# Optimization experiments

Hardware: AMD Instinct MI355X
Metric: run time of the kernel (lower is better)

Reference implementation:

```python
import jax, jax.numpy as jnp
import numpy as np

N, E = 20000, 640000
IN_CH, OUT_CH = 128, 64
HEADS = (4, 4)
NEG_SLOPE = 0.2


def _gat_layer(x, src, dst, edge_attr, edge_atten, W, a_src, a_dst, W_e, a_e, b, H, C, n_nodes):
    # x: [N, F_in] -> per-head features [N, H, C]
    xh = (x @ W).reshape(-1, H, C)
    alpha_src = jnp.sum(xh * a_src, axis=-1)          # [N, H]
    alpha_dst = jnp.sum(xh * a_dst, axis=-1)          # [N, H]
    eemb = (edge_attr @ W_e).reshape(-1, H, C)        # [E, H, C]
    alpha_e = jnp.sum(eemb * a_e, axis=-1)            # [E, H]
    alpha = alpha_src[src] + alpha_dst[dst] + alpha_e # [E, H]
    alpha = jax.nn.leaky_relu(alpha, NEG_SLOPE)
    # softmax over variable-degree neighborhoods (segments keyed by dst)
    amax = jax.ops.segment_max(alpha, dst, num_segments=n_nodes)
    alpha = jnp.exp(alpha - amax[dst])
    denom = jax.ops.segment_sum(alpha, dst, num_segments=n_nodes)
    alpha = alpha / (denom[dst] + 1e-16)
    msg = xh[src] * alpha[:, :, None]                 # [E, H, C]
    msg = msg * edge_atten[:, :, None]                # edge_atten: [E, 1] -> broadcast over H, C
    out = jax.ops.segment_sum(msg, dst, num_segments=n_nodes)
    out = out.reshape(n_nodes, H * C) + b
    return out, alpha


def setup_inputs() -> dict:
    key = jax.random.key(0)
    ks = jax.random.split(key, 16)
    H1, H2 = HEADS
    d1_in, d1_out = IN_CH, H1 * OUT_CH
    d2_in, d2_out = H1 * OUT_CH, H2 * OUT_CH
    s = lambda fi: 1.0 / np.sqrt(fi)
    inp = {
        "x": jax.random.normal(ks[0], (N, IN_CH), jnp.float32),
        "edge_index": jax.random.randint(ks[1], (2, E), 0, N, jnp.int64 if jax.config.jax_enable_x64 else jnp.int32),
        "batch": jnp.zeros((N,), jnp.int32),
        "edge_attr": jax.random.normal(ks[2], (E, 1), jnp.float32),
        "edge_atten": jax.random.uniform(ks[3], (E, 1), jnp.float32),
        # layer 1 params
        "W1": jax.random.normal(ks[4], (d1_in, d1_out), jnp.float32) * s(d1_in),
        "a_src1": jax.random.normal(ks[5], (H1, OUT_CH), jnp.float32) * s(OUT_CH),
        "a_dst1": jax.random.normal(ks[6], (H1, OUT_CH), jnp.float32) * s(OUT_CH),
        "W_e1": jax.random.normal(ks[7], (1, d1_out), jnp.float32),
        "a_e1": jax.random.normal(ks[8], (H1, OUT_CH), jnp.float32) * s(OUT_CH),
        "b1": jnp.zeros((d1_out,), jnp.float32),
        # layer 2 params
        "W2": jax.random.normal(ks[9], (d2_in, d2_out), jnp.float32) * s(d2_in),
        "a_src2": jax.random.normal(ks[10], (H2, OUT_CH), jnp.float32) * s(OUT_CH),
        "a_dst2": jax.random.normal(ks[11], (H2, OUT_CH), jnp.float32) * s(OUT_CH),
        "W_e2": jax.random.normal(ks[12], (1, d2_out), jnp.float32),
        "a_e2": jax.random.normal(ks[13], (H2, OUT_CH), jnp.float32) * s(OUT_CH),
        "b2": jnp.zeros((d2_out,), jnp.float32),
    }
    return inp


def reference(x, edge_index, batch, edge_attr, edge_atten,
              W1, a_src1, a_dst1, W_e1, a_e1, b1,
              W2, a_src2, a_dst2, W_e2, a_e2, b2):
    src, dst = edge_index[0], edge_index[1]
    h, w1 = _gat_layer(x, src, dst, edge_attr, edge_atten,
                       W1, a_src1, a_dst1, W_e1, a_e1, b1, HEADS[0], OUT_CH, N)
    h, w2 = _gat_layer(h, src, dst, edge_attr, edge_atten,
                       W2, a_src2, a_dst2, W_e2, a_e2, b2, HEADS[1], OUT_CH, N)
    return h, w1, w2
```

## Files before the change

kernel.cpp:

```cpp
#include <hip/hip_runtime.h>
#include <math.h>

#define NEG_SLOPE 0.2f
#define CAP 128
#define ST  136
#define NNODES 20000
#define NB 128

typedef short s16x8 __attribute__((ext_vector_type(8)));
typedef unsigned short us8 __attribute__((ext_vector_type(8)));
typedef float f32x4 __attribute__((ext_vector_type(4)));

__device__ __forceinline__ unsigned short f2bf(float f) {
    unsigned int u = __float_as_uint(f);
    return (unsigned short)((u + 0x7FFFu + ((u >> 16) & 1u)) >> 16);
}
__device__ __forceinline__ float bf2f(unsigned short s) {
    return __uint_as_float(((unsigned int)s) << 16);
}

__global__ __launch_bounds__(512) void hist_prep(const int* __restrict__ dst,
                                                 int* __restrict__ ghist,
                                                 int E, int chunk, int N, int histB,
                                                 const float* __restrict__ x,
                                                 const float* __restrict__ W1,
                                                 const float* __restrict__ W2,
                                                 const float* __restrict__ W_e1,
                                                 const float* __restrict__ a_e1,
                                                 const float* __restrict__ W_e2,
                                                 const float* __restrict__ a_e2,
                                                 unsigned short* __restrict__ xb16,
                                                 unsigned short* __restrict__ Wt1,
                                                 unsigned short* __restrict__ Wt2,
                                                 float* __restrict__ ce) {
    __shared__ int h[NNODES / 2];
    if ((int)blockIdx.x < histB) {
        const int b = blockIdx.x;
        const int NH = N >> 1;
        for (int i = threadIdx.x; i < NH; i += 512) h[i] = 0;
        __syncthreads();
        const int e0 = b * chunk;
        const int e1 = min(e0 + chunk, E);
        for (int e = e0 + (int)threadIdx.x; e < e1; e += 512) {
            int d = dst[e];
            atomicAdd(&h[d >> 1], 1 << ((d & 1) << 4));
        }
        __syncthreads();
        int2* out = (int2*)(ghist + (size_t)b * N);
        for (int i = threadIdx.x; i < NH; i += 512) {
            int v = h[i];
            out[i] = make_int2(v & 0xFFFF, ((unsigned)v) >> 16);
        }
    } else {
        const int p = (int)blockIdx.x - histB;
        const int gsz = 256 * 512;
        const int gid = p * 512 + (int)threadIdx.x;
        for (int i = gid; i < 128 * 256; i += gsz) {
            int k = i >> 8, n = i & 255;
            Wt1[n * 128 + k] = f2bf(W1[i]);
        }
        for (int i = gid; i < 256 * 256; i += gsz) {
            int k = i >> 8, n = i & 255;
            Wt2[n * 256 + k] = f2bf(W2[i]);
        }
        for (int i = gid; i < N * 32; i += gsz) {
            float4 f = ((const float4*)x)[i];
            ushort4 u = make_ushort4(f2bf(f.x), f2bf(f.y), f2bf(f.z), f2bf(f.w));
            ((ushort4*)xb16)[i] = u;
        }
        if (p < 2 && threadIdx.x < 256) {
            const float* We = p == 0 ? W_e1 : W_e2;
            const float* ae = p == 0 ? a_e1 : a_e2;
            int hh = threadIdx.x >> 6, c = threadIdx.x & 63;
            float pr = We[hh * 64 + c] * ae[hh * 64 + c];
#pragma unroll
            for (int off = 32; off > 0; off >>= 1) pr += __shfl_down(pr, off);
            if (c == 0) ce[p * 4 + hh] = pr;
        }
    }
}

__global__ __launch_bounds__(1024) void scan_kernel(const int* __restrict__ deg,
                                                    int* __restrict__ off, int N) {
    __shared__ int wsum[16];
    __shared__ int woff[16];
    __shared__ int s_carry, s_bt;
    if (threadIdx.x == 0) s_carry = 0;
    __syncthreads();
    const int lane = threadIdx.x & 63, wid = threadIdx.x >> 6;
    for (int base = 0; base < N; base += 4096) {
        int i0 = base + (int)threadIdx.x * 4;
        int v0 = (i0 + 0 < N) ? deg[i0 + 0] : 0;
        int v1 = (i0 + 1 < N) ? deg[i0 + 1] : 0;
        int v2 = (i0 + 2 < N) ? deg[i0 + 2] : 0;
        int v3 = (i0 + 3 < N) ? deg[i0 + 3] : 0;
        int tsum = v0 + v1 + v2 + v3;
        int incl = tsum;
#pragma unroll
        for (int ofs = 1; ofs < 64; ofs <<= 1) {
            int t = __shfl_up(incl, ofs);
            if (lane >= ofs) incl += t;
        }
        if (lane == 63) wsum[wid] = incl;
        __syncthreads();
        if (wid == 0) {
            int ws = (lane < 16) ? wsum[lane] : 0;
            int wincl = ws;
#pragma unroll
            for (int ofs = 1; ofs < 16; ofs <<= 1) {
                int t = __shfl_up(wincl, ofs);
                if (lane >= ofs) wincl += t;
            }
            if (lane < 16) woff[lane] = wincl - ws;
            if (lane == 15) s_bt = wincl;
        }
        __syncthreads();
        int e0 = s_carry + woff[wid] + incl - tsum;
        int e1 = e0 + v0, e2 = e1 + v1, e3 = e2 + v2;
        if (i0 + 0 < N) off[i0 + 0] = e0;
        if (i0 + 1 < N) off[i0 + 1] = e1;
        if (i0 + 2 < N) off[i0 + 2] = e2;
        if (i0 + 3 < N) off[i0 + 3] = e3;
        __syncthreads();
        if (threadIdx.x == 0) s_carry += s_bt;
        __syncthreads();
    }
    if (threadIdx.x == 0) off[N] = s_carry;
}

__device__ __forceinline__ void gemm_core(const unsigned short* __restrict__ A16,
                                          const unsigned short* __restrict__ Bt16,
                                          unsigned short* __restrict__ C16,
                                          const float* __restrict__ a_src,
                                          const float* __restrict__ a_dst,
                                          float* __restrict__ asrc,
                                          float* __restrict__ adst,
                                          int M, int K, int bx, int by,
                                          unsigned short (*As)[40],
                                          unsigned short (*Bs)[40]) {
    const int tid = threadIdx.x;
    const int w = tid >> 6, l = tid & 63;
    const int quad = l >> 4, m16 = l & 15;
    const int row0 = by * 128, col0 = bx * 64;

    f32x4 acc[2][4] = {};

    const int a_r = tid >> 1;
    const int a_k = (tid & 1) * 16;
    const int b_n = tid >> 2;
    const int b_k = (tid & 3) * 8;

    for (int k0 = 0; k0 < K; k0 += 32) {
        int gr = row0 + a_r; if (gr > M - 1) gr = M - 1;
        const unsigned short* ap = A16 + (size_t)gr * K + k0 + a_k;
        *(us8*)&As[a_r][a_k]     = *(const us8*)ap;
        *(us8*)&As[a_r][a_k + 8] = *(const us8*)(ap + 8);
        *(us8*)&Bs[b_n][b_k] = *(const us8*)(Bt16 + (size_t)(col0 + b_n) * K + k0 + b_k);
        __syncthreads();

        s16x8 af[2], bfr[4];
#pragma unroll
        for (int mt = 0; mt < 2; ++mt)
            af[mt] = *(const s16x8*)&As[w * 32 + mt * 16 + m16][quad * 8];
#pragma unroll
        for (int nt = 0; nt < 4; ++nt)
            bfr[nt] = *(const s16x8*)&Bs[nt * 16 + m16][quad * 8];
#pragma unroll
        for (int mt = 0; mt < 2; ++mt)
#pragma unroll
            for (int nt = 0; nt < 4; ++nt)
                acc[mt][nt] = __builtin_amdgcn_mfma_f32_16x16x32_bf16(af[mt], bfr[nt], acc[mt][nt], 0, 0, 0);
        __syncthreads();
    }

    const int h = bx;
    float was[4], wad[4];
#pragma unroll
    for (int nt = 0; nt < 4; ++nt) {
        int c = nt * 16 + m16;
        was[nt] = a_src[h * 64 + c];
        wad[nt] = a_dst[h * 64 + c];
    }

#pragma unroll
    for (int mt = 0; mt < 2; ++mt)
#pragma unroll
        for (int i = 0; i < 4; ++i) {
            int row = row0 + w * 32 + mt * 16 + quad * 4 + i;
            float ps = 0.f, pd = 0.f;
#pragma unroll
            for (int nt = 0; nt < 4; ++nt) {
                float v = acc[mt][nt][i];
                ps += v * was[nt];
                pd += v * wad[nt];
            }
#pragma unroll
            for (int ofs = 1; ofs < 16; ofs <<= 1) {
                ps += __shfl_xor(ps, ofs);
                pd += __shfl_xor(pd, ofs);
            }
            if (m16 == 0 && row < M) {
                asrc[(size_t)row * 4 + h] = ps;
                adst[(size_t)row * 4 + h] = pd;
            }
        }

#pragma unroll
    for (int mt = 0; mt < 2; ++mt)
#pragma unroll
        for (int nt = 0; nt < 4; ++nt) {
            int col = col0 + nt * 16 + m16;
#pragma unroll
            for (int i = 0; i < 4; ++i) {
                int row = row0 + w * 32 + mt * 16 + quad * 4 + i;
                if (row < M) C16[(size_t)row * 256 + col] = f2bf(acc[mt][nt][i]);
            }
        }
}

__global__ __launch_bounds__(256) void gemm1_scan(const unsigned short* __restrict__ A16,
                                                  const unsigned short* __restrict__ Bt16,
                                                  unsigned short* __restrict__ C16,
                                                  const float* __restrict__ a_src,
                                                  const float* __restrict__ a_dst,
                                                  float* __restrict__ asrc,
                                                  float* __restrict__ adst,
                                                  int M, int K, int gemmB,
                                                  int* __restrict__ ghist,
                                                  int* __restrict__ deg,
                                                  int N, int histB) {
    __shared__ unsigned short As[128][40];
    __shared__ unsigned short Bs[64][40];
    if ((int)blockIdx.x < gemmB) {
        gemm_core(A16, Bt16, C16, a_src, a_dst, asrc, adst, M, K,
                  blockIdx.x & 3, blockIdx.x >> 2, As, Bs);
    } else {
        int bin = ((int)blockIdx.x - gemmB) * 256 + (int)threadIdx.x;
        if (bin < N) {
            int run = 0;
            for (int b = 0; b < histB; b += 8) {
                int v[8];
#pragma unroll
                for (int j = 0; j < 8; ++j) v[j] = ghist[(b + j) * N + bin];
#pragma unroll
                for (int j = 0; j < 8; ++j) { ghist[(b + j) * N + bin] = run; run += v[j]; }
            }
            deg[bin] = run;
        }
    }
}

__global__ __launch_bounds__(1024) void fill2(const int* __restrict__ src,
                                              const int* __restrict__ dst,
                                              const float* __restrict__ edge_attr,
                                              const float* __restrict__ edge_atten,
                                              const int* __restrict__ off,
                                              const int* __restrict__ ghist,
                                              int4* __restrict__ rec,
                                              int E, int chunk, int N) {
    __shared__ int base[NNODES];
    const int b = blockIdx.x;
    const int* part = ghist + (size_t)b * N;
    for (int i = threadIdx.x; i < N; i += 1024) base[i] = off[i] + part[i];
    __syncthreads();
    const int e0 = b * chunk;
    const int e1 = min(e0 + chunk, E);
    for (int e = e0 + (int)threadIdx.x; e < e1; e += 1024) {
        int d = dst[e];
        int pos = atomicAdd(&base[d], 1);
        rec[pos] = make_int4(src[e], e, __float_as_int(edge_attr[e]),
                             __float_as_int(edge_atten[e]));
    }
}

__global__ __launch_bounds__(256) void node_fused(const int4* __restrict__ rec,
                                                  const int* __restrict__ off,
                                                  const float* __restrict__ asrc,
                                                  const float* __restrict__ adst,
                                                  const float* __restrict__ ce,
                                                  const unsigned short* __restrict__ xh16,
                                                  const float* __restrict__ bias,
                                                  float* __restrict__ w,
                                                  int write_w,
                                                  float* __restrict__ mxrc,
                                                  float* __restrict__ houtf,
                                                  unsigned short* __restrict__ hout16,
                                                  int N) {
    __shared__ float s_al[4][4][ST];
    __shared__ int s_src[4][CAP];
    const int wid = threadIdx.x >> 6;
    const int n = blockIdx.x * 4 + wid;
    if (n >= N) return;
    const int lane = threadIdx.x & 63;
    float* al = &s_al[wid][0][0];
    int* sv = s_src[wid];
    const int o0 = off[n], o1 = off[n + 1];
    const int deg = o1 - o0;

    const float4 c4 = *(const float4*)ce;
    const float4 ad4 = *(const float4*)(adst + (size_t)n * 4);

    if (deg <= 64) {
        int4 r; float4 a;
        a.x = a.y = a.z = a.w = -3.4e38f;
        if (lane < deg) {
            r = rec[o0 + lane];
            float ea = __int_as_float(r.z);
            const float4 as4 = *(const float4*)(asrc + (size_t)r.x * 4);
            a.x = as4.x + ad4.x + ea * c4.x;
            a.y = as4.y + ad4.y + ea * c4.y;
            a.z = as4.z + ad4.z + ea * c4.z;
            a.w = as4.w + ad4.w + ea * c4.w;
            a.x = a.x > 0.f ? a.x : NEG_SLOPE * a.x;
            a.y = a.y > 0.f ? a.y : NEG_SLOPE * a.y;
            a.z = a.z > 0.f ? a.z : NEG_SLOPE * a.z;
            a.w = a.w > 0.f ? a.w : NEG_SLOPE * a.w;
        }
        float4 mx = a;
#pragma unroll
        for (int ofs = 1; ofs < 64; ofs <<= 1) {
            mx.x = fmaxf(mx.x, __shfl_xor(mx.x, ofs));
            mx.y = fmaxf(mx.y, __shfl_xor(mx.y, ofs));
            mx.z = fmaxf(mx.z, __shfl_xor(mx.z, ofs));
            mx.w = fmaxf(mx.w, __shfl_xor(mx.w, ofs));
        }
        float4 ex = make_float4(0.f, 0.f, 0.f, 0.f);
        if (lane < deg) {
            ex.x = __expf(a.x - mx.x);
            ex.y = __expf(a.y - mx.y);
            ex.z = __expf(a.z - mx.z);
            ex.w = __expf(a.w - mx.w);
        }
        float4 sm = ex;
#pragma unroll
        for (int ofs = 1; ofs < 64; ofs <<= 1) {
            sm.x += __shfl_xor(sm.x, ofs);
            sm.y += __shfl_xor(sm.y, ofs);
            sm.z += __shfl_xor(sm.z, ofs);
            sm.w += __shfl_xor(sm.w, ofs);
        }
        float4 rc;
        rc.x = 1.f / (sm.x + 1e-16f);
        rc.y = 1.f / (sm.y + 1e-16f);
        rc.z = 1.f / (sm.z + 1e-16f);
        rc.w = 1.f / (sm.w + 1e-16f);
        if (mxrc && lane == 0) {
            *(float4*)(mxrc + (size_t)n * 8) = mx;
            *(float4*)(mxrc + (size_t)n * 8 + 4) = rc;
        }
        if (lane < deg) {
            float4 aln;
            aln.x = ex.x * rc.x;
            aln.y = ex.y * rc.y;
            aln.z = ex.z * rc.z;
            aln.w = ex.w * rc.w;
            if (write_w) *(float4*)(w + (size_t)r.y * 4) = aln;
            float att = __int_as_float(r.w);
            sv[lane] = r.x;
            al[0 * ST + lane] = aln.x * att;
            al[1 * ST + lane] = aln.y * att;
            al[2 * ST + lane] = aln.z * att;
            al[3 * ST + lane] = aln.w * att;
        }
    } else {
        float4 mx = make_float4(-3.4e38f, -3.4e38f, -3.4e38f, -3.4e38f);
        for (int idx = lane; idx < deg; idx += 64) {
            int4 r = rec[o0 + idx];
            float ea = __int_as_float(r.z);
            const float4 as4 = *(const float4*)(asrc + (size_t)r.x * 4);
            float4 a;
            a.x = as4.x + ad4.x + ea * c4.x;
            a.y = as4.y + ad4.y + ea * c4.y;
            a.z = as4.z + ad4.z + ea * c4.z;
            a.w = as4.w + ad4.w + ea * c4.w;
            a.x = a.x > 0.f ? a.x : NEG_SLOPE * a.x;
            a.y = a.y > 0.f ? a.y : NEG_SLOPE * a.y;
            a.z = a.z > 0.f ? a.z : NEG_SLOPE * a.z;
            a.w = a.w > 0.f ? a.w : NEG_SLOPE * a.w;
            if (idx < CAP) {
                sv[idx] = r.x;
                al[0 * ST + idx] = a.x;
                al[1 * ST + idx] = a.y;
                al[2 * ST + idx] = a.z;
                al[3 * ST + idx] = a.w;
            } else {
                *(float4*)(w + (size_t)r.y * 4) = a;
            }
            mx.x = fmaxf(mx.x, a.x);
            mx.y = fmaxf(mx.y, a.y);
            mx.z = fmaxf(mx.z, a.z);
            mx.w = fmaxf(mx.w, a.w);
        }
#pragma unroll
        for (int ofs = 1; ofs < 64; ofs <<= 1) {
            mx.x = fmaxf(mx.x, __shfl_xor(mx.x, ofs));
            mx.y = fmaxf(mx.y, __shfl_xor(mx.y, ofs));
            mx.z = fmaxf(mx.z, __shfl_xor(mx.z, ofs));
            mx.w = fmaxf(mx.w, __shfl_xor(mx.w, ofs));
        }
        float4 sm = make_float4(0.f, 0.f, 0.f, 0.f);
        for (int idx = lane; idx < deg; idx += 64) {
            float4 a;
            int espill = -1;
            if (idx < CAP) {
                a.x = al[0 * ST + idx];
                a.y = al[1 * ST + idx];
                a.z = al[2 * ST + idx];
                a.w = al[3 * ST + idx];
            } else {
                espill = rec[o0 + idx].y;
                a = *(const float4*)(w + (size_t)espill * 4);
            }
            a.x = __expf(a.x - mx.x);
            a.y = __expf(a.y - mx.y);
            a.z = __expf(a.z - mx.z);
            a.w = __expf(a.w - mx.w);
            if (idx < CAP) {
                al[0 * ST + idx] = a.x;
                al[1 * ST + idx] = a.y;
                al[2 * ST + idx] = a.z;
                al[3 * ST + idx] = a.w;
            } else {
                *(float4*)(w + (size_t)espill * 4) = a;
            }
            sm.x += a.x; sm.y += a.y; sm.z += a.z; sm.w += a.w;
        }
#pragma unroll
        for (int ofs = 1; ofs < 64; ofs <<= 1) {
            sm.x += __shfl_xor(sm.x, ofs);
            sm.y += __shfl_xor(sm.y, ofs);
            sm.z += __shfl_xor(sm.z, ofs);
            sm.w += __shfl_xor(sm.w, ofs);
        }
        float4 rc;
        rc.x = 1.f / (sm.x + 1e-16f);
        rc.y = 1.f / (sm.y + 1e-16f);
        rc.z = 1.f / (sm.z + 1e-16f);
        rc.w = 1.f / (sm.w + 1e-16f);
        if (mxrc && lane == 0) {
            *(float4*)(mxrc + (size_t)n * 8) = mx;
            *(float4*)(mxrc + (size_t)n * 8 + 4) = rc;
        }
        for (int idx = lane; idx < deg; idx += 64) {
            int4 r = rec[o0 + idx];
            float4 ex;
            if (idx < CAP) {
                ex.x = al[0 * ST + idx];
                ex.y = al[1 * ST + idx];
                ex.z = al[2 * ST + idx];
                ex.w = al[3 * ST + idx];
            } else {
                ex = *(const float4*)(w + (size_t)r.y * 4);
            }
            float4 aln;
            aln.x = ex.x * rc.x;
            aln.y = ex.y * rc.y;
            aln.z = ex.z * rc.z;
            aln.w = ex.w * rc.w;
            *(float4*)(w + (size_t)r.y * 4) = aln;
            if (idx < CAP) {
                float att = __int_as_float(r.w);
                al[0 * ST + idx] = aln.x * att;
                al[1 * ST + idx] = aln.y * att;
                al[2 * ST + idx] = aln.z * att;
                al[3 * ST + idx] = aln.w * att;
            }
        }
    }

    const int hh = lane >> 4;
    const float* alh = al + hh * ST;
    float4 a0 = *(const float4*)(bias + lane * 4);
    float4 a1 = make_float4(0.f, 0.f, 0.f, 0.f);
    float4 a2 = make_float4(0.f, 0.f, 0.f, 0.f);
    float4 a3 = make_float4(0.f, 0.f, 0.f, 0.f);
    const int kmax = deg < CAP ? deg : CAP;
    int k = 0;
    for (; k + 4 <= kmax; k += 4) {
        int4 s4 = *(const int4*)&sv[k];
        float4 cc = *(const float4*)&alh[k];
        ushort4 u0 = *((const ushort4*)(xh16 + (size_t)s4.x * 256) + lane);
        ushort4 u1 = *((const ushort4*)(xh16 + (size_t)s4.y * 256) + lane);
        ushort4 u2 = *((const ushort4*)(xh16 + (size_t)s4.z * 256) + lane);
        ushort4 u3 = *((const ushort4*)(xh16 + (size_t)s4.w * 256) + lane);
        a0.x += bf2f(u0.x) * cc.x; a0.y += bf2f(u0.y) * cc.x; a0.z += bf2f(u0.z) * cc.x; a0.w += bf2f(u0.w) * cc.x;
        a1.x += bf2f(u1.x) * cc.y; a1.y += bf2f(u1.y) * cc.y; a1.z += bf2f(u1.z) * cc.y; a1.w += bf2f(u1.w) * cc.y;
        a2.x += bf2f(u2.x) * cc.z; a2.y += bf2f(u2.y) * cc.z; a2.z += bf2f(u2.z) * cc.z; a2.w += bf2f(u2.w) * cc.z;
        a3.x += bf2f(u3.x) * cc.w; a3.y += bf2f(u3.y) * cc.w; a3.z += bf2f(u3.z) * cc.w; a3.w += bf2f(u3.w) * cc.w;
    }
    for (; k < kmax; ++k) {
        int s = sv[k];
        float sc = alh[k];
        ushort4 uv = *((const ushort4*)(xh16 + (size_t)s * 256) + lane);
        a0.x += bf2f(uv.x) * sc; a0.y += bf2f(uv.y) * sc;
        a0.z += bf2f(uv.z) * sc; a0.w += bf2f(uv.w) * sc;
    }
    for (k = CAP; k < deg; ++k) {
        int4 r = rec[o0 + k];
        float sc = w[(size_t)r.y * 4 + hh] * __int_as_float(r.w);
        ushort4 uv = *((const ushort4*)(xh16 + (size_t)r.x * 256) + lane);
        a0.x += bf2f(uv.x) * sc; a0.y += bf2f(uv.y) * sc;
        a0.z += bf2f(uv.z) * sc; a0.w += bf2f(uv.w) * sc;
    }
    float4 acc;
    acc.x = (a0.x + a1.x) + (a2.x + a3.x);
    acc.y = (a0.y + a1.y) + (a2.y + a3.y);
    acc.z = (a0.z + a1.z) + (a2.z + a3.z);
    acc.w = (a0.w + a1.w) + (a2.w + a3.w);
    if (houtf)  *(float4*)(houtf + (size_t)n * 256 + lane * 4) = acc;
    if (hout16) {
        ushort4 u = make_ushort4(f2bf(acc.x), f2bf(acc.y), f2bf(acc.z), f2bf(acc.w));
        *((ushort4*)(hout16 + (size_t)n * 256) + lane) = u;
    }
}

__global__ __launch_bounds__(256) void gemm2_w1(const unsigned short* __restrict__ A16,
                                                const unsigned short* __restrict__ Bt16,
                                                unsigned short* __restrict__ C16,
                                                const float* __restrict__ a_src,
                                                const float* __restrict__ a_dst,
                                                float* __restrict__ asrc2,
                                                float* __restrict__ adst2,
                                                int M, int K, int gemmB,
                                                const int* __restrict__ src,
                                                const int* __restrict__ dstp,
                                                const float* __restrict__ edge_attr,
                                                const float* __restrict__ asrc1,
                                                const float* __restrict__ adst1,
                                                const float* __restrict__ mxrc,
                                                const float* __restrict__ ce1,
                                                float* __restrict__ w1, int E) {
    __shared__ unsigned short As[128][40];
    __shared__ unsigned short Bs[64][40];
    if ((int)blockIdx.x < gemmB) {
        gemm_core(A16, Bt16, C16, a_src, a_dst, asrc2, adst2, M, K,
                  blockIdx.x & 3, blockIdx.x >> 2, As, Bs);
    } else {
        const int stride = ((int)gridDim.x - gemmB) * 256;
        const float4 c4 = *(const float4*)ce1;
        for (int e = ((int)blockIdx.x - gemmB) * 256 + (int)threadIdx.x; e < E; e += stride) {
            int s = src[e], d = dstp[e];
            float ea = edge_attr[e];
            const float4 as4 = *(const float4*)(asrc1 + (size_t)s * 4);
            const float4 ad4 = *(const float4*)(adst1 + (size_t)d * 4);
            float4 a;
            a.x = as4.x + ad4.x + ea * c4.x;
            a.y = as4.y + ad4.y + ea * c4.y;
            a.z = as4.z + ad4.z + ea * c4.z;
            a.w = as4.w + ad4.w + ea * c4.w;
            a.x = a.x > 0.f ? a.x : NEG_SLOPE * a.x;
            a.y = a.y > 0.f ? a.y : NEG_SLOPE * a.y;
            a.z = a.z > 0.f ? a.z : NEG_SLOPE * a.z;
            a.w = a.w > 0.f ? a.w : NEG_SLOPE * a.w;
            const float4 mx = *(const float4*)(mxrc + (size_t)d * 8);
            const float4 rc = *(const float4*)(mxrc + (size_t)d * 8 + 4);
            float4 o;
            o.x = __expf(a.x - mx.x) * rc.x;
            o.y = __expf(a.y - mx.y) * rc.y;
            o.z = __expf(a.z - mx.z) * rc.z;
            o.w = __expf(a.w - mx.w) * rc.w;
            *(float4*)(w1 + (size_t)e * 4) = o;
        }
    }
}

extern "C" void kernel_launch(void* const* d_in, const int* in_sizes, int n_in,
                              void* d_out, int out_size, void* d_ws, size_t ws_size,
                              hipStream_t stream) {
    const float* x          = (const float*)d_in[0];
    const int*   ei         = (const int*)d_in[1];
    const float* edge_attr  = (const float*)d_in[3];
    const float* edge_atten = (const float*)d_in[4];
    const float* W1     = (const float*)d_in[5];
    const float* a_src1 = (const float*)d_in[6];
    const float* a_dst1 = (const float*)d_in[7];
    const float* W_e1   = (const float*)d_in[8];
    const float* a_e1   = (const float*)d_in[9];
    const float* b1     = (const float*)d_in[10];
    const float* W2     = (const float*)d_in[11];
    const float* a_src2 = (const float*)d_in[12];
    const float* a_dst2 = (const float*)d_in[13];
    const float* W_e2   = (const float*)d_in[14];
    const float* a_e2   = (const float*)d_in[15];
    const float* b2     = (const float*)d_in[16];

    const int N = in_sizes[0] / 128;
    const int E = in_sizes[1] / 2;
    const int* srcp = ei;
    const int* dstp = ei + E;

    char* ws = (char*)d_ws;
    int4* rec             = (int4*)ws;            ws += (size_t)E * 16;
    unsigned short* xh16  = (unsigned short*)ws;  ws += (size_t)N * 256 * 2;
    unsigned short* h116  = (unsigned short*)ws;  ws += (size_t)N * 256 * 2;
    unsigned short* Wt1   = (unsigned short*)ws;  ws += (size_t)256 * 128 * 2;
    unsigned short* Wt2   = (unsigned short*)ws;  ws += (size_t)256 * 256 * 2;
    float* asrc   = (float*)ws;                   ws += (size_t)N * 4 * 4;
    float* adst   = (float*)ws;                   ws += (size_t)N * 4 * 4;
    float* asrc2  = (float*)ws;                   ws += (size_t)N * 4 * 4;
    float* adst2  = (float*)ws;                   ws += (size_t)N * 4 * 4;
    float* mxrc   = (float*)ws;                   ws += (size_t)N * 8 * 4;
    float* ce     = (float*)ws;                   ws += 32;
    int* deg    = (int*)ws;                       ws += (size_t)N * 4;
    int* off    = (int*)ws;                       ws += (size_t)(N + 1) * 4;
    int* ghist  = (int*)ws;                       ws += (size_t)NB * N * 4;

    unsigned short* xb16 = h116;

    float* hout2 = (float*)d_out;
    float* w1    = hout2 + (size_t)N * 256;
    float* w2    = w1 + (size_t)E * 4;

    const int chunk = (E + NB - 1) / NB;
    const int gb = (N + 3) / 4;
    const int rows = (N + 127) / 128;
    const int gemmB = 4 * rows;
    const int scanB = (N + 255) / 256;
    const int wB = 512;

    hist_prep<<<NB + 256, 512, 0, stream>>>(dstp, ghist, E, chunk, N, NB,
                                            x, W1, W2, W_e1, a_e1, W_e2, a_e2,
                                            xb16, Wt1, Wt2, ce);
    gemm1_scan<<<gemmB + scanB, 256, 0, stream>>>(xb16, Wt1, xh16, a_src1, a_dst1,
                                                  asrc, adst, N, 128, gemmB,
                                                  ghist, deg, N, NB);
    scan_kernel<<<1, 1024, 0, stream>>>(deg, off, N);
    fill2<<<NB, 1024, 0, stream>>>(srcp, dstp, edge_attr, edge_atten, off, ghist,
                                   rec, E, chunk, N);
    node_fused<<<gb, 256, 0, stream>>>(rec, off, asrc, adst, ce, xh16, b1, w1,
                                       0, mxrc, (float*)nullptr, h116, N);
    gemm2_w1<<<gemmB + wB, 256, 0, stream>>>(h116, Wt2, xh16, a_src2, a_dst2,
                                             asrc2, adst2, N, 256, gemmB,
                                             srcp, dstp, edge_attr,
                                             asrc, adst, mxrc, ce, w1, E);
    node_fused<<<gb, 256, 0, stream>>>(rec, off, asrc2, adst2, ce + 4, xh16, b2, w2,
                                       1, (float*)nullptr, hout2,
                                       (unsigned short*)nullptr, N);
}
```

Baseline: 255.9 us.

## Co-schedule layer-1 GEMM with CSR fill using byte-packed shared counters

Moves the column scan of the per-block histogram into its own small kernel and launches the layer-1 GEMM blocks together with the CSR fill blocks in one grid, so the GEMM overlaps the edge scatter instead of overlapping the column scan. The fill uses 8-bit packed per-node counters in 20KB of shared memory instead of a 20000-int array, which lowers LDS use and allows more resident blocks. Each edge now reads off and part from global memory instead of a prebuilt shared base array. The aggregation loop in node_fused is also unrolled to 8 neighbours per step to issue more gathers at once. The packed counters assume fewer than 256 edges per node per chunk, and N must be divisible by 4.

Result: slower. 266.3 us (+4.1%).

```diff
diff --git a/kernel.cpp b/kernel.cpp
--- a/kernel.cpp
+++ b/kernel.cpp
@@ -80,6 +80,23 @@
     }
 }
 
+__global__ __launch_bounds__(256) void colscan(int* __restrict__ ghist,
+                                               int* __restrict__ deg,
+                                               int N, int histB) {
+    int bin = blockIdx.x * 256 + (int)threadIdx.x;
+    if (bin < N) {
+        int run = 0;
+        for (int b = 0; b < histB; b += 8) {
+            int v[8];
+#pragma unroll
+            for (int j = 0; j < 8; ++j) v[j] = ghist[(b + j) * N + bin];
+#pragma unroll
+            for (int j = 0; j < 8; ++j) { ghist[(b + j) * N + bin] = run; run += v[j]; }
+        }
+        deg[bin] = run;
+    }
+}
+
 __global__ __launch_bounds__(1024) void scan_kernel(const int* __restrict__ deg,
                                                     int* __restrict__ off, int N) {
     __shared__ int wsum[16];
@@ -218,58 +235,45 @@
         }
 }
 
-__global__ __launch_bounds__(256) void gemm1_scan(const unsigned short* __restrict__ A16,
-                                                  const unsigned short* __restrict__ Bt16,
-                                                  unsigned short* __restrict__ C16,
-                                                  const float* __restrict__ a_src,
-                                                  const float* __restrict__ a_dst,
-                                                  float* __restrict__ asrc,
-                                                  float* __restrict__ adst,
-                                                  int M, int K, int gemmB,
-                                                  int* __restrict__ ghist,
-                                                  int* __restrict__ deg,
-                                                  int N, int histB) {
-    __shared__ unsigned short As[128][40];
-    __shared__ unsigned short Bs[64][40];
+__global__ __launch_bounds__(256) void gemm1_fill3(const unsigned short* __restrict__ A16,
+                                                   const unsigned short* __restrict__ Bt16,
+                                                   unsigned short* __restrict__ C16,
+                                                   const float* __restrict__ a_src,
+                                                   const float* __restrict__ a_dst,
+                                                   float* __restrict__ asrc,
+                                                   float* __restrict__ adst,
+                                                   int M, int K, int gemmB,
+                                                   const int* __restrict__ src,
+                                                   const int* __restrict__ dst,
+                                                   const float* __restrict__ edge_attr,
+                                                   const float* __restrict__ edge_atten,
+                                                   const int* __restrict__ off,
+                                                   const int* __restrict__ ghist,
+                                                   int4* __restrict__ rec,
+                                                   int E, int chunk, int N) {
+    __shared__ int smem[5120];
     if ((int)blockIdx.x < gemmB) {
         gemm_core(A16, Bt16, C16, a_src, a_dst, asrc, adst, M, K,
-                  blockIdx.x & 3, blockIdx.x >> 2, As, Bs);
+                  blockIdx.x & 3, blockIdx.x >> 2,
+                  (unsigned short (*)[40])smem,
+                  (unsigned short (*)[40])((char*)smem + 10240));
     } else {
-        int bin = ((int)blockIdx.x - gemmB) * 256 + (int)threadIdx.x;
-        if (bin < N) {
-            int run = 0;
-            for (int b = 0; b < histB; b += 8) {
-                int v[8];
-#pragma unroll
-                for (int j = 0; j < 8; ++j) v[j] = ghist[(b + j) * N + bin];
-#pragma unroll
-                for (int j = 0; j < 8; ++j) { ghist[(b + j) * N + bin] = run; run += v[j]; }
-            }
-            deg[bin] = run;
-        }
-    }
-}
-
-__global__ __launch_bounds__(1024) void fill2(const int* __restrict__ src,
-                                              const int* __restrict__ dst,
-                                              const float* __restrict__ edge_attr,
-                                              const float* __restrict__ edge_atten,
-                                              const int* __restrict__ off,
-                                              const int* __restrict__ ghist,
-                                              int4* __restrict__ rec,
-                                              int E, int chunk, int N) {
-    __shared__ int base[NNODES];
-    const int b = blockIdx.x;
-    const int* part = ghist + (size_t)b * N;
-    for (int i = threadIdx.x; i < N; i += 1024) base[i] = off[i] + part[i];
-    __syncthreads();
-    const int e0 = b * chunk;
-    const int e1 = min(e0 + chunk, E);
-    for (int e = e0 + (int)threadIdx.x; e < e1; e += 1024) {
-        int d = dst[e];
-        int pos = atomicAdd(&base[d], 1);
-        rec[pos] = make_int4(src[e], e, __float_as_int(edge_attr[e]),
-                             __float_as_int(edge_atten[e]));
+        const int b = (int)blockIdx.x - gemmB;
+        const int NW = N >> 2;
+        for (int i = threadIdx.x; i < NW; i += 256) smem[i] = 0;
+        __syncthreads();
+        const int* part = ghist + (size_t)b * N;
+        const int e0 = b * chunk;
+        const int e1 = min(e0 + chunk, E);
+        for (int e = e0 + (int)threadIdx.x; e < e1; e += 256) {
+            int d = dst[e];
+            int sh = (d & 3) << 3;
+            unsigned old = atomicAdd((unsigned*)&smem[d >> 2], 1u << sh);
+            int rank = (old >> sh) & 0xFF;
+            int pos = off[d] + part[d] + rank;
+            rec[pos] = make_int4(src[e], e, __float_as_int(edge_attr[e]),
+                                 __float_as_int(edge_atten[e]));
+        }
     }
 }
 
@@ -472,10 +476,31 @@
     const float* alh = al + hh * ST;
     float4 a0 = *(const float4*)(bias + lane * 4);
     float4 a1 = make_float4(0.f, 0.f, 0.f, 0.f);
-    float4 a2 = make_float4(0.f, 0.f, 0.f, 0.f);
-    float4 a3 = make_float4(0.f, 0.f, 0.f, 0.f);
+    float4 a2 = a1, a3 = a1;
     const int kmax = deg < CAP ? deg : CAP;
     int k = 0;
+    for (; k + 8 <= kmax; k += 8) {
+        int4 s4a = *(const int4*)&sv[k];
+        int4 s4b = *(const int4*)&sv[k + 4];
+        float4 ca = *(const float4*)&alh[k];
+        float4 cb = *(const float4*)&alh[k + 4];
+        ushort4 u0 = *((const ushort4*)(xh16 + (size_t)s4a.x * 256) + lane);
+        ushort4 u1 = *((const ushort4*)(xh16 + (size_t)s4a.y * 256) + lane);
+        ushort4 u2 = *((const ushort4*)(xh16 + (size_t)s4a.z * 256) + lane);
+        ushort4 u3 = *((const ushort4*)(xh16 + (size_t)s4a.w * 256) + lane);
+        ushort4 u4 = *((const ushort4*)(xh16 + (size_t)s4b.x * 256) + lane);
+        ushort4 u5 = *((const ushort4*)(xh16 + (size_t)s4b.y * 256) + lane);
+        ushort4 u6 = *((const ushort4*)(xh16 + (size_t)s4b.z * 256) + lane);
+        ushort4 u7 = *((const ushort4*)(xh16 + (size_t)s4b.w * 256) + lane);
+        a0.x += bf2f(u0.x) * ca.x; a0.y += bf2f(u0.y) * ca.x; a0.z += bf2f(u0.z) * ca.x; a0.w += bf2f(u0.w) * ca.x;
+        a1.x += bf2f(u1.x) * ca.y; a1.y += bf2f(u1.y) * ca.y; a1.z += bf2f(u1.z) * ca.y; a1.w += bf2f(u1.w) * ca.y;
+        a2.x += bf2f(u2.x) * ca.z; a2.y += bf2f(u2.y) * ca.z; a2.z += bf2f(u2.z) * ca.z; a2.w += bf2f(u2.w) * ca.z;
+        a3.x += bf2f(u3.x) * ca.w; a3.y += bf2f(u3.y) * ca.w; a3.z += bf2f(u3.z) * ca.w; a3.w += bf2f(u3.w) * ca.w;
+        a0.x += bf2f(u4.x) * cb.x; a0.y += bf2f(u4.y) * cb.x; a0.z += bf2f(u4.z) * cb.x; a0.w += bf2f(u4.w) * cb.x;
+        a1.x += bf2f(u5.x) * cb.y; a1.y += bf2f(u5.y) * cb.y; a1.z += bf2f(u5.z) * cb.y; a1.w += bf2f(u5.w) * cb.y;
+        a2.x += bf2f(u6.x) * cb.z; a2.y += bf2f(u6.y) * cb.z; a2.z += bf2f(u6.z) * cb.z; a2.w += bf2f(u6.w) * cb.z;
+        a3.x += bf2f(u7.x) * cb.w; a3.y += bf2f(u7.y) * cb.w; a3.z += bf2f(u7.z) * cb.w; a3.w += bf2f(u7.w) * cb.w;
+    }
     for (; k + 4 <= kmax; k += 4) {
         int4 s4 = *(const int4*)&sv[k];
         float4 cc = *(const float4*)&alh[k];
@@ -621,12 +646,12 @@
     hist_prep<<<NB + 256, 512, 0, stream>>>(dstp, ghist, E, chunk, N, NB,
                                             x, W1, W2, W_e1, a_e1, W_e2, a_e2,
                                             xb16, Wt1, Wt2, ce);
-    gemm1_scan<<<gemmB + scanB, 256, 0, stream>>>(xb16, Wt1, xh16, a_src1, a_dst1,
-                                                  asrc, adst, N, 128, gemmB,
-                                                  ghist, deg, N, NB);
+    colscan<<<scanB, 256, 0, stream>>>(ghist, deg, N, NB);
     scan_kernel<<<1, 1024, 0, stream>>>(deg, off, N);
-    fill2<<<NB, 1024, 0, stream>>>(srcp, dstp, edge_attr, edge_atten, off, ghist,
-                                   rec, E, chunk, N);
+    gemm1_fill3<<<gemmB + NB, 256, 0, stream>>>(xb16, Wt1, xh16, a_src1, a_dst1,
+                                                asrc, adst, N, 128, gemmB,
+                                                srcp, dstp, edge_attr, edge_atten,
+                                                off, ghist, rec, E, chunk, N);
     node_fused<<<gb, 256, 0, stream>>>(rec, off, asrc, adst, ce, xh16, b1, w1,
                                        0, mxrc, (float*)nullptr, h116, N);
     gemm2_w1<<<gemmB + wB, 256, 0, stream>>>(h116, Wt2, xh16, a_src2, a_dst2,
```
